# Optimization experiments

Measured on AMD Instinct MI355X. Metric: run time of the kernel, lower is better.

## Reference

```python
import jax, jax.numpy as jnp
import numpy as np
import math

N_QUBITS = 8
N_LAYERS = 4
DIM = 2 ** N_QUBITS


def _ry(theta):
    # theta: (...,) -> (..., 2, 2) real RY matrix, cast to complex64
    c, s = jnp.cos(theta / 2), jnp.sin(theta / 2)
    g = jnp.stack([jnp.stack([c, -s], -1), jnp.stack([s, c], -1)], -2)
    return g.astype(jnp.complex64)


def _apply_1q(psi, gate, q):
    # psi: (B, 2**n); gate: (2,2) shared or (B,2,2) per-sample; qubit q (wire 0 = MSB)
    B = psi.shape[0]
    L, R = 2 ** q, 2 ** (N_QUBITS - q - 1)
    s = psi.reshape(B, L, 2, R)
    if gate.ndim == 2:
        s = jnp.einsum('ij,bljr->blir', gate, s)
    else:
        s = jnp.einsum('bij,bljr->blir', gate, s)
    return s.reshape(B, DIM)


def _cnot(psi, c):
    # CNOT on adjacent wires (c, c+1): swap |10> <-> |11> on that 4-dim block
    B = psi.shape[0]
    L, R = 2 ** c, 2 ** (N_QUBITS - c - 2)
    s = psi.reshape(B, L, 4, R)
    s = s[:, :, jnp.array([0, 1, 3, 2]), :]
    return s.reshape(B, DIM)


def setup_inputs() -> dict:
    key = jax.random.key(0)
    kx, kw = jax.random.split(key)
    B = 65536
    x = jax.random.uniform(kx, (B, N_QUBITS), jnp.float32, -math.pi, math.pi)
    bound = 1.0 / math.sqrt(N_QUBITS)
    weights = jax.random.uniform(kw, (N_LAYERS, N_QUBITS, 2), jnp.float32, -bound, bound)
    return {"x": x, "weights": weights}


def reference(x, weights):
    B = x.shape[0]
    # |0...0> initial state
    psi = jnp.zeros((B, DIM), jnp.complex64).at[:, 0].set(1.0)
    # angle encoding: RY(x_i) on wire i (per-sample gates)
    enc = _ry(x)  # (B, n, 2, 2)
    for q in range(N_QUBITS):
        psi = _apply_1q(psi, enc[:, q], q)
    # variational layers: RY(w[l,i,0]) then RZ(w[l,i,1]) on each wire, then CNOT chain
    for l in range(N_LAYERS):
        ry = _ry(weights[l, :, 0])  # (n, 2, 2)
        tz = weights[l, :, 1]
        ez_m = jnp.exp(-0.5j * tz.astype(jnp.complex64))  # e^{-i theta/2}
        ez_p = jnp.exp(0.5j * tz.astype(jnp.complex64))   # e^{+i theta/2}
        phases = jnp.stack([ez_m, ez_p], axis=-1)  # (n, 2) diag of RZ
        g = phases[:, :, None] * ry  # (n,2,2) = RZ @ RY (fused rotation)
        for q in range(N_QUBITS):
            psi = _apply_1q(psi, g[q], q)
        for c in range(N_QUBITS - 1):
            psi = _cnot(psi, c)
    # PauliZ expectations per wire
    p = psi.real ** 2 + psi.imag ** 2  # (B, DIM)
    exps = []
    for q in range(N_QUBITS):
        pq = p.reshape(B, 2 ** q, 2, -1).sum(axis=(1, 3))  # (B, 2)
        exps.append(pq[:, 0] - pq[:, 1])
    return jnp.stack(exps, axis=1)  # (B, n_qubits)
```

## Files before the change

kernel.cpp:

```cpp
#include <hip/hip_runtime.h>


typedef _Float16 half8  __attribute__((ext_vector_type(8)));
typedef float    float4v __attribute__((ext_vector_type(4)));
typedef unsigned int uint2v __attribute__((ext_vector_type(2)));
typedef unsigned int uint4v __attribute__((ext_vector_type(4)));

#define MEMFENCE() __asm__ volatile("" ::: "memory")

__device__ __forceinline__ unsigned pk2(float a, float b) {
  auto v = __builtin_amdgcn_cvt_pkrtz(a, b);
  return __builtin_bit_cast(unsigned, v);
}
__device__ __forceinline__ float rdlane(float v, int l) {
  return __builtin_bit_cast(float, __builtin_amdgcn_readlane(__builtin_bit_cast(int, v), l));
}
__device__ __forceinline__ unsigned sw8u(unsigned v) {
  return (unsigned)__builtin_amdgcn_mov_dpp((int)v, 0x128, 0xf, 0xf, false);
}
__device__ __forceinline__ float sw8f(float v) {
  return __builtin_bit_cast(float,
      __builtin_amdgcn_mov_dpp(__builtin_bit_cast(int, v), 0x128, 0xf, 0xf, false));
}
__device__ __forceinline__ int tauf(int l) {
  int y = l ^ (((l >> 3) & 1) << 2);
  y ^= ((y >> 2) & 1) << 1;
  y ^= (y >> 1) & 1;
  return y;
}

__launch_bounds__(256, 2)
__global__ void qmain(const float* __restrict__ x, const float* __restrict__ w,
                      float* __restrict__ out) {
  __shared__ __align__(16) unsigned char smem[32768];
  const int tid = threadIdx.x;
  const int lane = tid & 63, wv = tid >> 6;
  const int quad = lane >> 4, n = lane & 15;

  {
    const int t = wv;
    int mr = n ^ ((n >> 1) & 1);
    mr ^= ((mr >> 2) & 1) << 1;
    mr ^= ((mr >> 3) & 1) << 2;
    float cS[8], sS[8], zcS[8], zsS[8];
#pragma unroll
    for (int qq = 0; qq < 8; ++qq) {
      float th = w[(t * 8 + qq) * 2 + 0];
      float tz = w[(t * 8 + qq) * 2 + 1];
      __sincosf(0.5f * th, &sS[qq], &cS[qq]);
      __sincosf(0.5f * tz, &zsS[qq], &zcS[qq]);
    }
    union { _Float16 h[8]; half8 v; } bLR, bLI, bRR, bRI;
#pragma unroll
    for (int ci = 0; ci < 4; ++ci) {
      const int kp = quad * 4 + ci;
      float hr = 1.f, hi = 0.f;
#pragma unroll
      for (int j = 0; j < 4; ++j) {
        int rb = (mr >> (3 - j)) & 1, cb = (kp >> (3 - j)) & 1;
        float ryv = (rb == cb) ? cS[j] : (rb ? sS[j] : -sS[j]);
        float ar = zcS[j] * ryv;
        float ai = (rb ? zsS[j] : -zsS[j]) * ryv;
        float nr = hr * ar - hi * ai, ni = hr * ai + hi * ar;
        hr = nr; hi = ni;
      }
      bLR.h[2 * ci] = (_Float16)hr;  bLR.h[2 * ci + 1] = (_Float16)(-hi);
      bLI.h[2 * ci] = (_Float16)hi;  bLI.h[2 * ci + 1] = (_Float16)hr;
      int yk = tauf(kp);
      float wr = 1.f, wi = 0.f;
#pragma unroll
      for (int j = 0; j < 4; ++j) {
        int rb = (n >> (3 - j)) & 1, cb = (yk >> (3 - j)) & 1;
        float ryv = (rb == cb) ? cS[4 + j] : (rb ? sS[4 + j] : -sS[4 + j]);
        float ar = zcS[4 + j] * ryv;
        float ai = (rb ? zsS[4 + j] : -zsS[4 + j]) * ryv;
        float nr = wr * ar - wi * ai, ni = wr * ai + wi * ar;
        wr = nr; wi = ni;
      }
      bRR.h[2 * ci] = (_Float16)wr;  bRR.h[2 * ci + 1] = (_Float16)(-wi);
      bRI.h[2 * ci] = (_Float16)wi;  bRI.h[2 * ci + 1] = (_Float16)wr;
    }
    half8* FB = (half8*)smem;
    FB[(t * 4 + 0) * 64 + lane] = bLR.v;
    FB[(t * 4 + 1) * 64 + lane] = bLI.v;
    FB[(t * 4 + 2) * 64 + lane] = bRR.v;
    FB[(t * 4 + 3) * 64 + lane] = bRI.v;
  }
  __syncthreads();
  half8 BLR[4], BLI[4], BRR[4], BRI[4];
#pragma unroll
  for (int t = 0; t < 4; ++t) {
    const half8* FB = (const half8*)smem;
    BLR[t] = FB[(t * 4 + 0) * 64 + lane];
    BLI[t] = FB[(t * 4 + 1) * 64 + lane];
    BRR[t] = FB[(t * 4 + 2) * 64 + lane];
    BRI[t] = FB[(t * 4 + 3) * 64 + lane];
  }
  __syncthreads();

  half8 sf[8];
#pragma unroll
  for (int c = 0; c < 8; ++c) {
    union { _Float16 h[8]; half8 v; } sg;
#pragma unroll
    for (int jj = 0; jj < 8; ++jj) {
      int u = (quad & 1) * 8 + jj;
      int y = tauf(2 * c + (quad >> 1));
      float sv = 0.f;
      if (n < 8) {
        int bit = (n < 4) ? ((u >> (3 - n)) & 1) : ((y >> (7 - n)) & 1);
        sv = bit ? -1.f : 1.f;
      }
      sg.h[jj] = (_Float16)sv;
    }
    sf[c] = sg.v;
  }

  unsigned char* smp = smem + wv * 8192;
  const unsigned pWg = (unsigned)(2 * n + (quad >> 1));
  const unsigned pWlo = (unsigned)((quad & 1) * 8);
  const int e0 = (blockIdx.x * 4 + wv) * 32;
  const float4v zz = {0.f, 0.f, 0.f, 0.f};
  const int ytau = tauf(n);

  const float* xp = x + (size_t)e0 * 8;
  float x0 = xp[lane], x1 = xp[64 + lane], x2 = xp[128 + lane], x3 = xp[192 + lane];
  float c0, s0, c1, s1, c2, s2, c3, s3;
  __sincosf(0.5f * x0, &s0, &c0);
  __sincosf(0.5f * x1, &s1, &c1);
  __sincosf(0.5f * x2, &s2, &c2);
  __sincosf(0.5f * x3, &s3, &c3);

  for (int g = 0; g < 2; ++g) {
    const int base = e0 + g * 16;
    const float CA = g ? c2 : c0, SA = g ? s2 : s0;
    const float CB = g ? c3 : c1, SB = g ? s3 : s1;

#pragma unroll
    for (int i = 0; i < 4; ++i) {
      uint4v st[4];
#pragma unroll
      for (int h = 0; h < 4; ++h) {
        const int e = 4 * i + h;
        const float cs = (e < 8) ? CA : CB;
        const float sn = (e < 8) ? SA : SB;
        const int lb = (e & 7) * 8;
        float cq[8], sq[8];
#pragma unroll
        for (int q = 0; q < 8; ++q) { cq[q] = rdlane(cs, lb + q); sq[q] = rdlane(sn, lb + q); }
        float f0 = (quad & 2) ? sq[0] : cq[0];
        float f1 = (quad & 1) ? sq[1] : cq[1];
        float f4 = (ytau & 8) ? sq[4] : cq[4];
        float f5 = (ytau & 4) ? sq[5] : cq[5];
        float f6 = (ytau & 2) ? sq[6] : cq[6];
        float f7 = (ytau & 1) ? sq[7] : cq[7];
        float pb = f0 * f1 * f4 * f5 * f6 * f7;
        st[h][0] = pk2(pb * cq[2] * cq[3], 0.f);
        st[h][1] = pk2(pb * cq[2] * sq[3], 0.f);
        st[h][2] = pk2(pb * sq[2] * cq[3], 0.f);
        st[h][3] = pk2(pb * sq[2] * sq[3], 0.f);
      }

#pragma unroll
      for (int t = 0; t < 4; ++t) {
        float4v xr[4], xi[4];
#pragma unroll
        for (int c = 0; c < 4; ++c) {
          half8 A = __builtin_bit_cast(half8, st[c]);
          xr[c] = __builtin_amdgcn_mfma_f32_16x16x32_f16(A, BLR[t], zz, 0, 0, 0);
          xi[c] = __builtin_amdgcn_mfma_f32_16x16x32_f16(A, BLI[t], zz, 0, 0, 0);
        }
        uint4v X[4];
#pragma unroll
        for (int c = 0; c < 4; ++c) {
          X[c][0] = pk2(xr[c][0], xi[c][0]);
          X[c][1] = pk2(xr[c][1], xi[c][1]);
          X[c][2] = pk2(xr[c][2], xi[c][2]);
          X[c][3] = pk2(xr[c][3], xi[c][3]);
        }
        float4v yr[4], yi[4];
#pragma unroll
        for (int c = 0; c < 4; ++c) {
          half8 XA = __builtin_bit_cast(half8, X[c]);
          yr[c] = __builtin_amdgcn_mfma_f32_16x16x32_f16(XA, BRR[t], zz, 0, 0, 0);
          yi[c] = __builtin_amdgcn_mfma_f32_16x16x32_f16(XA, BRI[t], zz, 0, 0, 0);
        }
        if (t < 3) {
#pragma unroll
          for (int c = 0; c < 4; ++c) {
            st[c][0] = pk2(yr[c][0], yi[c][0]);
            st[c][1] = sw8u(pk2(yr[c][1], yi[c][1]));
            st[c][2] = pk2(yr[c][2], yi[c][2]);
            st[c][3] = sw8u(pk2(yr[c][3], yi[c][3]));
          }
        } else {
          MEMFENCE();
#pragma unroll
          for (int c = 0; c < 4; ++c) {
            float r1 = sw8f(yr[c][1]), i1 = sw8f(yi[c][1]);
            float r3 = sw8f(yr[c][3]), i3 = sw8f(yi[c][3]);
            float p0 = yr[c][0] * yr[c][0] + yi[c][0] * yi[c][0];
            float p1 = r1 * r1 + i1 * i1;
            float p2 = yr[c][2] * yr[c][2] + yi[c][2] * yi[c][2];
            float p3 = r3 * r3 + i3 * i3;
            const unsigned e = (unsigned)(4 * i + c);
            unsigned pOff = e * 512u + ((pWg ^ (e & 7u)) << 4) + pWlo;
            uint2v v = { pk2(p0, p1), pk2(p2, p3) };
            *(uint2v*)(smp + pOff) = v;
          }
          MEMFENCE();
        }
      }
    }

    float4v acc = zz;
    MEMFENCE();
#pragma unroll
    for (int c = 0; c < 8; ++c) {
      unsigned pR = (unsigned)(n * 512 +
                               ((((unsigned)(c * 4 + quad)) ^ (unsigned)(n & 7)) << 4));
      half8 pbv = *(const half8*)(smp + pR);
      acc = __builtin_amdgcn_mfma_f32_16x16x32_f16(sf[c], pbv, acc, 0, 0, 0);
    }
    MEMFENCE();
    if (quad < 2) {
      float4v* o = (float4v*)(out + (size_t)(base + n) * 8 + quad * 4);
      *o = acc;
    }
  }
}

extern "C" void kernel_launch(void* const* d_in, const int* in_sizes, int n_in,
                              void* d_out, int out_size, void* d_ws, size_t ws_size,
                              hipStream_t stream) {
  const float* x = (const float*)d_in[0];
  const float* w = (const float*)d_in[1];
  float* out = (float*)d_out;
  qmain<<<dim3(512), dim3(256), 0, stream>>>(x, w, out);
}
```

Before: 75.72 us.

## Halve per-wave batch, move sign matrix to LDS, raise occupancy to four blocks

Each wave now processes 16 samples instead of 32, the grid doubles to 1024 blocks, and the launch bounds ask for 4 blocks per CU. The sign-pattern fragments for the final reduction are kept in shared memory instead of 8 half8 registers, and the inner batch of state chunks shrinks from 4 to 2, so register use should drop and occupancy rise, giving more latency hiding. In exchange, MFMA chains per wave are shorter and less interleaved, shared memory per block grows to 40 KB, and there are extra LDS reads in the epilogue.

```diff
diff --git a/kernel.cpp b/kernel.cpp
--- a/kernel.cpp
+++ b/kernel.cpp
@@ -29,10 +29,10 @@
   return y;
 }
 
-__launch_bounds__(256, 2)
+__launch_bounds__(256, 4)
 __global__ void qmain(const float* __restrict__ x, const float* __restrict__ w,
                       float* __restrict__ out) {
-  __shared__ __align__(16) unsigned char smem[32768];
+  __shared__ __align__(16) unsigned char smem[40960];
   const int tid = threadIdx.x;
   const int lane = tid & 63, wv = tid >> 6;
   const int quad = lane >> 4, n = lane & 15;
@@ -80,7 +80,7 @@
       bRR.h[2 * ci] = (_Float16)wr;  bRR.h[2 * ci + 1] = (_Float16)(-wi);
       bRI.h[2 * ci] = (_Float16)wi;  bRI.h[2 * ci + 1] = (_Float16)wr;
     }
-    half8* FB = (half8*)smem;
+    half8* FB = (half8*)(smem + 8192);
     FB[(t * 4 + 0) * 64 + lane] = bLR.v;
     FB[(t * 4 + 1) * 64 + lane] = bLI.v;
     FB[(t * 4 + 2) * 64 + lane] = bRR.v;
@@ -90,15 +90,12 @@
   half8 BLR[4], BLI[4], BRR[4], BRI[4];
 #pragma unroll
   for (int t = 0; t < 4; ++t) {
-    const half8* FB = (const half8*)smem;
+    const half8* FB = (const half8*)(smem + 8192);
     BLR[t] = FB[(t * 4 + 0) * 64 + lane];
     BLI[t] = FB[(t * 4 + 1) * 64 + lane];
     BRR[t] = FB[(t * 4 + 2) * 64 + lane];
     BRI[t] = FB[(t * 4 + 3) * 64 + lane];
   }
-  __syncthreads();
-
-  half8 sf[8];
 #pragma unroll
   for (int c = 0; c < 8; ++c) {
     union { _Float16 h[8]; half8 v; } sg;
@@ -113,120 +110,113 @@
       }
       sg.h[jj] = (_Float16)sv;
     }
-    sf[c] = sg.v;
-  }
-
-  unsigned char* smp = smem + wv * 8192;
+    *(half8*)(smem + c * 1024 + lane * 16) = sg.v;
+  }
+  __syncthreads();
+
+  unsigned char* smp = smem + 8192 + wv * 8192;
   const unsigned pWg = (unsigned)(2 * n + (quad >> 1));
   const unsigned pWlo = (unsigned)((quad & 1) * 8);
-  const int e0 = (blockIdx.x * 4 + wv) * 32;
+  const int e0 = (blockIdx.x * 4 + wv) * 16;
   const float4v zz = {0.f, 0.f, 0.f, 0.f};
   const int ytau = tauf(n);
 
   const float* xp = x + (size_t)e0 * 8;
-  float x0 = xp[lane], x1 = xp[64 + lane], x2 = xp[128 + lane], x3 = xp[192 + lane];
-  float c0, s0, c1, s1, c2, s2, c3, s3;
-  __sincosf(0.5f * x0, &s0, &c0);
-  __sincosf(0.5f * x1, &s1, &c1);
-  __sincosf(0.5f * x2, &s2, &c2);
-  __sincosf(0.5f * x3, &s3, &c3);
-
-  for (int g = 0; g < 2; ++g) {
-    const int base = e0 + g * 16;
-    const float CA = g ? c2 : c0, SA = g ? s2 : s0;
-    const float CB = g ? c3 : c1, SB = g ? s3 : s1;
-
-#pragma unroll
-    for (int i = 0; i < 4; ++i) {
-      uint4v st[4];
-#pragma unroll
-      for (int h = 0; h < 4; ++h) {
-        const int e = 4 * i + h;
-        const float cs = (e < 8) ? CA : CB;
-        const float sn = (e < 8) ? SA : SB;
-        const int lb = (e & 7) * 8;
-        float cq[8], sq[8];
-#pragma unroll
-        for (int q = 0; q < 8; ++q) { cq[q] = rdlane(cs, lb + q); sq[q] = rdlane(sn, lb + q); }
-        float f0 = (quad & 2) ? sq[0] : cq[0];
-        float f1 = (quad & 1) ? sq[1] : cq[1];
-        float f4 = (ytau & 8) ? sq[4] : cq[4];
-        float f5 = (ytau & 4) ? sq[5] : cq[5];
-        float f6 = (ytau & 2) ? sq[6] : cq[6];
-        float f7 = (ytau & 1) ? sq[7] : cq[7];
-        float pb = f0 * f1 * f4 * f5 * f6 * f7;
-        st[h][0] = pk2(pb * cq[2] * cq[3], 0.f);
-        st[h][1] = pk2(pb * cq[2] * sq[3], 0.f);
-        st[h][2] = pk2(pb * sq[2] * cq[3], 0.f);
-        st[h][3] = pk2(pb * sq[2] * sq[3], 0.f);
-      }
-
-#pragma unroll
-      for (int t = 0; t < 4; ++t) {
-        float4v xr[4], xi[4];
-#pragma unroll
-        for (int c = 0; c < 4; ++c) {
-          half8 A = __builtin_bit_cast(half8, st[c]);
-          xr[c] = __builtin_amdgcn_mfma_f32_16x16x32_f16(A, BLR[t], zz, 0, 0, 0);
-          xi[c] = __builtin_amdgcn_mfma_f32_16x16x32_f16(A, BLI[t], zz, 0, 0, 0);
+  float xA = xp[lane], xB = xp[64 + lane];
+  float CA, SA, CB, SB;
+  __sincosf(0.5f * xA, &SA, &CA);
+  __sincosf(0.5f * xB, &SB, &CB);
+
+  for (int i = 0; i < 8; ++i) {
+    uint4v st[2];
+#pragma unroll
+    for (int h = 0; h < 2; ++h) {
+      const int e = 2 * i + h;
+      const float cs = (i < 4) ? CA : CB;
+      const float sn = (i < 4) ? SA : SB;
+      const int lb = (e & 7) * 8;
+      float cq[8], sq[8];
+#pragma unroll
+      for (int q = 0; q < 8; ++q) { cq[q] = rdlane(cs, lb + q); sq[q] = rdlane(sn, lb + q); }
+      float f0 = (quad & 2) ? sq[0] : cq[0];
+      float f1 = (quad & 1) ? sq[1] : cq[1];
+      float f4 = (ytau & 8) ? sq[4] : cq[4];
+      float f5 = (ytau & 4) ? sq[5] : cq[5];
+      float f6 = (ytau & 2) ? sq[6] : cq[6];
+      float f7 = (ytau & 1) ? sq[7] : cq[7];
+      float pb = f0 * f1 * f4 * f5 * f6 * f7;
+      st[h][0] = pk2(pb * cq[2] * cq[3], 0.f);
+      st[h][1] = pk2(pb * cq[2] * sq[3], 0.f);
+      st[h][2] = pk2(pb * sq[2] * cq[3], 0.f);
+      st[h][3] = pk2(pb * sq[2] * sq[3], 0.f);
+    }
+
+#pragma unroll
+    for (int t = 0; t < 4; ++t) {
+      float4v xr[2], xi[2];
+#pragma unroll
+      for (int c = 0; c < 2; ++c) {
+        half8 A = __builtin_bit_cast(half8, st[c]);
+        xr[c] = __builtin_amdgcn_mfma_f32_16x16x32_f16(A, BLR[t], zz, 0, 0, 0);
+        xi[c] = __builtin_amdgcn_mfma_f32_16x16x32_f16(A, BLI[t], zz, 0, 0, 0);
+      }
+      uint4v X[2];
+#pragma unroll
+      for (int c = 0; c < 2; ++c) {
+        X[c][0] = pk2(xr[c][0], xi[c][0]);
+        X[c][1] = pk2(xr[c][1], xi[c][1]);
+        X[c][2] = pk2(xr[c][2], xi[c][2]);
+        X[c][3] = pk2(xr[c][3], xi[c][3]);
+      }
+      float4v yr[2], yi[2];
+#pragma unroll
+      for (int c = 0; c < 2; ++c) {
+        half8 XA = __builtin_bit_cast(half8, X[c]);
+        yr[c] = __builtin_amdgcn_mfma_f32_16x16x32_f16(XA, BRR[t], zz, 0, 0, 0);
+        yi[c] = __builtin_amdgcn_mfma_f32_16x16x32_f16(XA, BRI[t], zz, 0, 0, 0);
+      }
+      if (t < 3) {
+#pragma unroll
+        for (int c = 0; c < 2; ++c) {
+          st[c][0] = pk2(yr[c][0], yi[c][0]);
+          st[c][1] = sw8u(pk2(yr[c][1], yi[c][1]));
+          st[c][2] = pk2(yr[c][2], yi[c][2]);
+          st[c][3] = sw8u(pk2(yr[c][3], yi[c][3]));
         }
-        uint4v X[4];
-#pragma unroll
-        for (int c = 0; c < 4; ++c) {
-          X[c][0] = pk2(xr[c][0], xi[c][0]);
-          X[c][1] = pk2(xr[c][1], xi[c][1]);
-          X[c][2] = pk2(xr[c][2], xi[c][2]);
-          X[c][3] = pk2(xr[c][3], xi[c][3]);
+      } else {
+        MEMFENCE();
+#pragma unroll
+        for (int c = 0; c < 2; ++c) {
+          float r1 = sw8f(yr[c][1]), i1 = sw8f(yi[c][1]);
+          float r3 = sw8f(yr[c][3]), i3 = sw8f(yi[c][3]);
+          float p0 = yr[c][0] * yr[c][0] + yi[c][0] * yi[c][0];
+          float p1 = r1 * r1 + i1 * i1;
+          float p2 = yr[c][2] * yr[c][2] + yi[c][2] * yi[c][2];
+          float p3 = r3 * r3 + i3 * i3;
+          const unsigned e = (unsigned)(2 * i + c);
+          unsigned pOff = e * 512u + ((pWg ^ (e & 7u)) << 4) + pWlo;
+          uint2v v = { pk2(p0, p1), pk2(p2, p3) };
+          *(uint2v*)(smp + pOff) = v;
         }
-        float4v yr[4], yi[4];
-#pragma unroll
-        for (int c = 0; c < 4; ++c) {
-          half8 XA = __builtin_bit_cast(half8, X[c]);
-          yr[c] = __builtin_amdgcn_mfma_f32_16x16x32_f16(XA, BRR[t], zz, 0, 0, 0);
-          yi[c] = __builtin_amdgcn_mfma_f32_16x16x32_f16(XA, BRI[t], zz, 0, 0, 0);
-        }
-        if (t < 3) {
-#pragma unroll
-          for (int c = 0; c < 4; ++c) {
-            st[c][0] = pk2(yr[c][0], yi[c][0]);
-            st[c][1] = sw8u(pk2(yr[c][1], yi[c][1]));
-            st[c][2] = pk2(yr[c][2], yi[c][2]);
-            st[c][3] = sw8u(pk2(yr[c][3], yi[c][3]));
-          }
-        } else {
-          MEMFENCE();
-#pragma unroll
-          for (int c = 0; c < 4; ++c) {
-            float r1 = sw8f(yr[c][1]), i1 = sw8f(yi[c][1]);
-            float r3 = sw8f(yr[c][3]), i3 = sw8f(yi[c][3]);
-            float p0 = yr[c][0] * yr[c][0] + yi[c][0] * yi[c][0];
-            float p1 = r1 * r1 + i1 * i1;
-            float p2 = yr[c][2] * yr[c][2] + yi[c][2] * yi[c][2];
-            float p3 = r3 * r3 + i3 * i3;
-            const unsigned e = (unsigned)(4 * i + c);
-            unsigned pOff = e * 512u + ((pWg ^ (e & 7u)) << 4) + pWlo;
-            uint2v v = { pk2(p0, p1), pk2(p2, p3) };
-            *(uint2v*)(smp + pOff) = v;
-          }
-          MEMFENCE();
-        }
-      }
-    }
-
-    float4v acc = zz;
-    MEMFENCE();
-#pragma unroll
-    for (int c = 0; c < 8; ++c) {
-      unsigned pR = (unsigned)(n * 512 +
-                               ((((unsigned)(c * 4 + quad)) ^ (unsigned)(n & 7)) << 4));
-      half8 pbv = *(const half8*)(smp + pR);
-      acc = __builtin_amdgcn_mfma_f32_16x16x32_f16(sf[c], pbv, acc, 0, 0, 0);
-    }
-    MEMFENCE();
-    if (quad < 2) {
-      float4v* o = (float4v*)(out + (size_t)(base + n) * 8 + quad * 4);
-      *o = acc;
-    }
+        MEMFENCE();
+      }
+    }
+  }
+
+  float4v acc = zz;
+  MEMFENCE();
+#pragma unroll
+  for (int c = 0; c < 8; ++c) {
+    half8 sfv = *(const half8*)(smem + c * 1024 + lane * 16);
+    unsigned pR = (unsigned)(n * 512 +
+                             ((((unsigned)(c * 4 + quad)) ^ (unsigned)(n & 7)) << 4));
+    half8 pbv = *(const half8*)(smp + pR);
+    acc = __builtin_amdgcn_mfma_f32_16x16x32_f16(sfv, pbv, acc, 0, 0, 0);
+  }
+  MEMFENCE();
+  if (quad < 2) {
+    float4v* o = (float4v*)(out + (size_t)(e0 + n) * 8 + quad * 4);
+    *o = acc;
   }
 }
 
@@ -236,5 +226,5 @@
   const float* x = (const float*)d_in[0];
   const float* w = (const float*)d_in[1];
   float* out = (float*)d_out;
-  qmain<<<dim3(512), dim3(256), 0, stream>>>(x, w, out);
-}
+  qmain<<<dim3(1024), dim3(256), 0, stream>>>(x, w, out);
+}
```

New measurement: 80.52 us. 6.3% more time.
